# Kernel optimization log

Hardware: AMD Instinct MI355X
Metric: run time of the kernel (lower is better)

Reference implementation:

```python
import jax, jax.numpy as jnp
import numpy as np

N = 100000      # nodes
E = 1600000     # edges (before self loops)
H = 64          # hidden channels (per-head out dim, concat=False)
HEADS = 2
L = 2           # num GAT blocks
IN = 64
OUT = 10
B = 64          # graphs in batch
SLOPE = 0.2     # LeakyReLU negative slope (GATv2Conv default)
EPS = 1e-5      # BatchNorm eps


def setup_inputs() -> dict:
    key = jax.random.key(0)
    ks = jax.random.split(key, 10)
    s = 0.05
    x = jax.random.normal(ks[0], (N, IN), jnp.float32)
    edge_index = jax.random.randint(ks[1], (2, E), 0, N, dtype=jnp.int64)
    batch = jnp.sort(jax.random.randint(ks[2], (N,), 0, B, dtype=jnp.int64))
    W_enc = jax.random.normal(ks[3], (IN, H), jnp.float32) * s
    b_enc = jnp.zeros((H,), jnp.float32)
    Wl = jax.random.normal(ks[4], (L, H, HEADS * H), jnp.float32) * s
    bl = jnp.zeros((L, HEADS * H), jnp.float32)
    Wr = jax.random.normal(ks[5], (L, H, HEADS * H), jnp.float32) * s
    br = jnp.zeros((L, HEADS * H), jnp.float32)
    att = jax.random.normal(ks[6], (L, HEADS, H), jnp.float32) * s
    bias = jnp.zeros((L, H), jnp.float32)
    gamma = jnp.ones((L, H), jnp.float32)
    beta = jnp.zeros((L, H), jnp.float32)
    W_cls = jax.random.normal(ks[7], (H, OUT), jnp.float32) * s
    b_cls = jnp.zeros((OUT,), jnp.float32)
    return dict(x=x, edge_index=edge_index, batch=batch, W_enc=W_enc, b_enc=b_enc,
                Wl=Wl, bl=bl, Wr=Wr, br=br, att=att, bias=bias,
                gamma=gamma, beta=beta, W_cls=W_cls, b_cls=b_cls)


def reference(x, edge_index, batch, W_enc, b_enc, Wl, bl, Wr, br, att, bias,
              gamma, beta, W_cls, b_cls):
    # add self loops (GATv2Conv default add_self_loops=True)
    loops = jnp.arange(N, dtype=edge_index.dtype)
    ei = jnp.concatenate([edge_index, jnp.stack([loops, loops])], axis=1)
    src, dst = ei[0], ei[1]

    h = x @ W_enc + b_enc                                   # [N, H] atom encoder (Linear)
    for l in range(L):
        xl = (h @ Wl[l] + bl[l]).reshape(N, HEADS, H)       # source transform
        xr = (h @ Wr[l] + br[l]).reshape(N, HEADS, H)       # target transform
        # GATv2: e_uv = a^T LeakyReLU(W_l x_u + W_r x_v)
        z = jax.nn.leaky_relu(xl[src] + xr[dst], SLOPE)     # [E', heads, H]
        e = jnp.einsum('ehc,hc->eh', z, att[l])             # [E', heads]
        # segment softmax over incoming edges of each dst node
        m = jax.ops.segment_max(e, dst, num_segments=N)     # [N, heads]
        ex = jnp.exp(e - m[dst])
        den = jax.ops.segment_sum(ex, dst, num_segments=N)
        alpha = ex / den[dst]                               # [E', heads]
        out = jax.ops.segment_sum(xl[src] * alpha[:, :, None], dst, num_segments=N)
        h_new = out.mean(axis=1) + bias[l]                  # concat=False: mean over heads
        # BatchNorm1d (batch statistics) -> ReLU; dropout=0
        mu = h_new.mean(axis=0)
        var = h_new.var(axis=0)
        h = jax.nn.relu((h_new - mu) * jax.lax.rsqrt(var + EPS) * gamma[l] + beta[l])

    # global mean pool over graphs
    cnt = jax.ops.segment_sum(jnp.ones((N,), h.dtype), batch, num_segments=B)
    g = jax.ops.segment_sum(h, batch, num_segments=B) / jnp.maximum(cnt, 1.0)[:, None]
    return g @ W_cls + b_cls                                # [B, OUT]
```

## Files before the change

kernel.cpp:

```cpp
#include <hip/hip_runtime.h>

#define N_NODES 100000
#define E_EDGES 1600000
#define EP_EDGES (E_EDGES + N_NODES)
#define SLOPE 0.2f
#define BN_EPS 1e-5f
#define NB 8
#define NODES_PER_B 12500
#define NREP 32
#define SUBREG 8192
#define SCATTER_BLKS ((EP_EDGES + 255) / 256)
#define NBLK ((N_NODES + 63) / 64)

typedef _Float16 h2 __attribute__((ext_vector_type(2)));
typedef _Float16 v4h __attribute__((ext_vector_type(4)));
typedef _Float16 v8h __attribute__((ext_vector_type(8)));
typedef float v4f __attribute__((ext_vector_type(4)));

#if defined(__has_builtin)
#if __has_builtin(__builtin_amdgcn_fdot2)
#define HAVE_FDOT2 1
#endif
#endif

__device__ __forceinline__ float fdot2f(h2 a, h2 b, float c) {
#ifdef HAVE_FDOT2
    return __builtin_amdgcn_fdot2(a, b, c, false);
#else
    return c + (float)a[0] * (float)b[0] + (float)a[1] * (float)b[1];
#endif
}
__device__ __forceinline__ h2 bch2(unsigned u) { return __builtin_bit_cast(h2, u); }
__device__ __forceinline__ unsigned bcu(h2 v) { return __builtin_bit_cast(unsigned, v); }
__device__ __forceinline__ h2 habs2(h2 z) {
    return __builtin_bit_cast(h2, (unsigned)(__builtin_bit_cast(unsigned, z) & 0x7fff7fffu));
}
__device__ __forceinline__ h2 shflx_h2(h2 a, int o) {
    return __builtin_bit_cast(h2, __shfl_xor(__builtin_bit_cast(int, a), o, 64));
}

template <int CTRL>
__device__ __forceinline__ float dpp_add_step(float v) {
    int r = __builtin_amdgcn_update_dpp(0, __float_as_int(v), CTRL, 0xF, 0xF, false);
    return v + __int_as_float(r);
}
__device__ __forceinline__ float rowsum16(float v) {
    v = dpp_add_step<0x128>(v);
    v = dpp_add_step<0x124>(v);
    v = dpp_add_step<0x122>(v);
    v = dpp_add_step<0x121>(v);
    return v;
}

__device__ __forceinline__ void bucket_scatter_body(int bid, const int* __restrict__ src,
                                                    const int* __restrict__ dst,
                                                    int* __restrict__ gcur, unsigned* __restrict__ ebuf) {
    int i = bid * 256 + threadIdx.x;
    int rep = bid & (NREP - 1);
    bool active = i < EP_EDGES;
    int s = 0, d = 0;
    if (i < E_EDGES) { s = src[i]; d = dst[i]; }
    else if (active) { s = i - E_EDGES; d = s; }
    int b = active ? (int)((unsigned)d / NODES_PER_B) : NB;
    unsigned long long lt = (1ull << (threadIdx.x & 63)) - 1ull;
    int rank = 0;
    unsigned long long mymask = 0;
#pragma unroll
    for (int bb = 0; bb < NB; ++bb) {
        unsigned long long m = __ballot(b == bb);
        if (b == bb) { rank = __popcll(m & lt); mymask = m; }
    }
    int leader = mymask ? (__ffsll((long long)mymask) - 1) : 0;
    int lanebit = threadIdx.x & 63;
    int chunkbase = 0;
    if (active && lanebit == leader)
        chunkbase = atomicAdd(&gcur[rep * NB + b], (int)__popcll(mymask));
    chunkbase = __shfl(chunkbase, leader, 64);
    if (active) {
        unsigned dl = (unsigned)d - (unsigned)b * NODES_PER_B;
        ebuf[(size_t)(rep * NB + b) * SUBREG + chunkbase + rank] = (dl << 17) | (unsigned)s;
    }
}

__device__ __forceinline__ void fuse_enc_pack0(const float* __restrict__ We, const float* __restrict__ be,
                                               const float* __restrict__ Wl, const float* __restrict__ bl,
                                               const float* __restrict__ Wr, const float* __restrict__ br,
                                               _Float16* __restrict__ Wfrag0, float* __restrict__ bias0,
                                               float (*sWe)[64], float* sbe) {
    int t = threadIdx.x;
    for (int i = t; i < 4096; i += 256) sWe[i & 63][i >> 6] = We[i];
    if (t < 64) sbe[t] = be[t];
    __syncthreads();
    int j = t & 127, side = t >> 7;
    const float* W  = side ? Wr : Wl;
    const float* bb = side ? br : bl;
    float acc[64];
#pragma unroll
    for (int k = 0; k < 64; ++k) acc[k] = 0.f;
    float bacc = bb[j];
    for (int m = 0; m < 64; ++m) {
        float wv = W[m * 128 + j];
        bacc += sbe[m] * wv;
#pragma unroll
        for (int k = 0; k < 64; ++k) acc[k] += sWe[m][k] * wv;
    }
    int ncolg = (side << 7) | j;
    int w = ncolg >> 6, nt = (ncolg >> 4) & 3, lp = ncolg & 15;
#pragma unroll
    for (int k = 0; k < 64; ++k) {
        int kt = k >> 5;
        int l = (((k >> 3) & 3) << 4) | lp;
        int jj = k & 7;
        Wfrag0[((((w * 4 + nt) * 2 + kt)) << 9) + (l << 3) + jj] = (_Float16)acc[k];
    }
    bias0[ncolg] = bacc;
}

__device__ __forceinline__ void pack1_body(const float* __restrict__ WL, const float* __restrict__ WR,
                                           const float* __restrict__ bL, const float* __restrict__ bR,
                                           _Float16* __restrict__ Wfrag, float* __restrict__ bias_all) {
    int t = threadIdx.x;
    for (int i = t; i < 16384; i += 256) {
        int j = i & 7, l = (i >> 3) & 63, kt = (i >> 9) & 1, nt = (i >> 10) & 3, w = i >> 12;
        int ncol = w * 64 + nt * 16 + (l & 15);
        int k = kt * 32 + (l >> 4) * 8 + j;
        int side = ncol >> 7, colW = ncol & 127;
        Wfrag[i] = (_Float16)((side ? WR : WL)[k * 128 + colW]);
    }
    if (t < 256) {
        int side = t >> 7, colW = t & 127;
        bias_all[t] = (side ? bR : bL)[colW];
    }
}

__global__ __launch_bounds__(256) void scatter_fuse(const int* __restrict__ src, const int* __restrict__ dst,
                                                    int* __restrict__ gcur, unsigned* __restrict__ ebuf,
                                                    const float* __restrict__ We, const float* __restrict__ be,
                                                    const float* __restrict__ Wl, const float* __restrict__ bl,
                                                    const float* __restrict__ Wr, const float* __restrict__ br,
                                                    _Float16* __restrict__ Wfrag0, float* __restrict__ bias0,
                                                    _Float16* __restrict__ Wfrag1, float* __restrict__ bias1) {
    __shared__ float sWe[64][64];
    __shared__ float sbe[64];
    if (blockIdx.x == 0)
        fuse_enc_pack0(We, be, Wl, bl, Wr, br, Wfrag0, bias0, sWe, sbe);
    else if (blockIdx.x == 1)
        pack1_body(Wl + 64 * 128, Wr + 64 * 128, bl + 128, br + 128, Wfrag1, bias1);
    else
        bucket_scatter_body(blockIdx.x - 2, src, dst, gcur, ebuf);
}

template <int BN>
__device__ __forceinline__ void mfma_body(int mb, const void* __restrict__ hin,
                                          const _Float16* __restrict__ Wfrag,
                                          const float* __restrict__ bias_all,
                                          const float* __restrict__ bns, const float* __restrict__ gamma,
                                          const float* __restrict__ beta,
                                          unsigned short* __restrict__ xl, unsigned short* __restrict__ xr,
                                          char* smem, float* ssc, float* ssh) {
    int t = threadIdx.x;
    int w = t >> 6, l = t & 63;
    if (BN) {
        if (t < 64) {
            float s = 0.f, sq = 0.f;
#pragma unroll
            for (int r = 0; r < 8; ++r) { s += bns[r * 128 + t]; sq += bns[r * 128 + 64 + t]; }
            float mu = s * (1.f / N_NODES);
            float var = sq * (1.f / N_NODES) - mu * mu;
            float sc = gamma[t] * rsqrtf(var + BN_EPS);
            ssc[t] = sc; ssh[t] = beta[t] - mu * sc;
        }
        __syncthreads();
    }
    int base = mb * 64;
    if (BN == 0) {
#pragma unroll
        for (int pass = 0; pass < 4; ++pass) {
            int idx = t + pass * 256;
            int node = idx >> 4, q4 = idx & 15;
            int gnode = base + node;
            float4 v = make_float4(0.f, 0.f, 0.f, 0.f);
            if (gnode < N_NODES) v = *(const float4*)((const float*)hin + (size_t)gnode * 64 + q4 * 4);
            v4h p = {(_Float16)v.x, (_Float16)v.y, (_Float16)v.z, (_Float16)v.w};
            int byte = (node * 128 + q4 * 8) ^ ((node & 7) << 4);
            *(v4h*)(smem + byte) = p;
        }
    } else {
#pragma unroll
        for (int pass = 0; pass < 2; ++pass) {
            int idx = t + pass * 256;
            int node = idx >> 3, q8 = idx & 7;
            int gnode = base + node;
            uint4 u = make_uint4(0, 0, 0, 0);
            if (gnode < N_NODES) u = *(const uint4*)((const unsigned short*)hin + (size_t)gnode * 64 + q8 * 8);
            int c0 = q8 * 8;
            h2 p0 = bch2(u.x), p1 = bch2(u.y), p2 = bch2(u.z), p3 = bch2(u.w);
            float a, b;
            a = fmaxf((float)p0[0] * ssc[c0 + 0] + ssh[c0 + 0], 0.f);
            b = fmaxf((float)p0[1] * ssc[c0 + 1] + ssh[c0 + 1], 0.f);
            p0 = (h2){(_Float16)a, (_Float16)b};
            a = fmaxf((float)p1[0] * ssc[c0 + 2] + ssh[c0 + 2], 0.f);
            b = fmaxf((float)p1[1] * ssc[c0 + 3] + ssh[c0 + 3], 0.f);
            p1 = (h2){(_Float16)a, (_Float16)b};
            a = fmaxf((float)p2[0] * ssc[c0 + 4] + ssh[c0 + 4], 0.f);
            b = fmaxf((float)p2[1] * ssc[c0 + 5] + ssh[c0 + 5], 0.f);
            p2 = (h2){(_Float16)a, (_Float16)b};
            a = fmaxf((float)p3[0] * ssc[c0 + 6] + ssh[c0 + 6], 0.f);
            b = fmaxf((float)p3[1] * ssc[c0 + 7] + ssh[c0 + 7], 0.f);
            p3 = (h2){(_Float16)a, (_Float16)b};
            int byte = (node * 128 + q8 * 16) ^ ((node & 7) << 4);
            *(uint4*)(smem + byte) = make_uint4(bcu(p0), bcu(p1), bcu(p2), bcu(p3));
        }
    }
    v8h bfr[4][2];
    float biasv[4];
#pragma unroll
    for (int nt = 0; nt < 4; ++nt) {
#pragma unroll
        for (int kt = 0; kt < 2; ++kt)
            bfr[nt][kt] = *(const v8h*)(Wfrag + ((((w * 4 + nt) * 2 + kt) << 9) + (l << 3)));
        biasv[nt] = bias_all[w * 64 + nt * 16 + (l & 15)];
    }
    __syncthreads();
    v4f acc[4][4];
#pragma unroll
    for (int mt = 0; mt < 4; ++mt)
#pragma unroll
        for (int nt = 0; nt < 4; ++nt)
            acc[mt][nt] = (v4f){0.f, 0.f, 0.f, 0.f};
#pragma unroll
    for (int mt = 0; mt < 4; ++mt) {
        int node = mt * 16 + (l & 15);
        int swz = (node & 7) << 4;
        int b0 = (node * 128 + ((l >> 4) << 4)) ^ swz;
        int b1 = (node * 128 + 64 + ((l >> 4) << 4)) ^ swz;
        v8h a0 = *(const v8h*)(smem + b0);
        v8h a1 = *(const v8h*)(smem + b1);
#pragma unroll
        for (int nt = 0; nt < 4; ++nt) {
            acc[mt][nt] = __builtin_amdgcn_mfma_f32_16x16x32_f16(a0, bfr[nt][0], acc[mt][nt], 0, 0, 0);
            acc[mt][nt] = __builtin_amdgcn_mfma_f32_16x16x32_f16(a1, bfr[nt][1], acc[mt][nt], 0, 0, 0);
        }
    }
    _Float16* sOut = (_Float16*)(smem + 8192);
    __syncthreads();
#pragma unroll
    for (int mt = 0; mt < 4; ++mt) {
#pragma unroll
        for (int nt = 0; nt < 4; ++nt) {
            int ncol = (w << 6) + (nt << 4) + (l & 15);
            int side = ncol >> 7, head = (ncol >> 6) & 1, c = ncol & 63;
            int oidx = ((c >> 2) << 3) + (head << 2) + (c & 3);
            int obase = side * 128 + oidx;
#pragma unroll
            for (int j = 0; j < 4; ++j) {
                int node = mt * 16 + ((l >> 4) << 2) + j;
                sOut[node * 256 + obase] = (_Float16)(acc[mt][nt][j] + biasv[nt]);
            }
        }
    }
    __syncthreads();
#pragma unroll
    for (int pass = 0; pass < 8; ++pass) {
        int idx = t + pass * 256;
        int node = idx >> 5, wi = idx & 31;
        int gnode = base + node;
        if (gnode < N_NODES) {
            int side = wi >> 4, o16 = wi & 15;
            uint4 val = *(const uint4*)(sOut + node * 256 + side * 128 + o16 * 8);
            unsigned short* dstp = side ? xr : xl;
            *(uint4*)(dstp + (size_t)gnode * 128 + o16 * 8) = val;
        }
    }
}

__global__ __launch_bounds__(256) void deg_mfma0(const int* __restrict__ gcur,
                                                 const unsigned* __restrict__ ebuf,
                                                 int* __restrict__ deg,
                                                 const float* __restrict__ x,
                                                 const _Float16* __restrict__ Wfrag0,
                                                 const float* __restrict__ bias0,
                                                 unsigned short* __restrict__ xl, unsigned short* __restrict__ xr) {
    __shared__ __align__(16) char smem[40960];
    __shared__ float ssc[64], ssh[64];
    if (blockIdx.x < NREP * NB) {
        unsigned* ldeg4 = (unsigned*)smem;
        int b = blockIdx.x & (NB - 1), rep = blockIdx.x >> 3;
        for (int j = threadIdx.x; j < NODES_PER_B / 4 + 1; j += 256) ldeg4[j] = 0;
        __syncthreads();
        int cnt = gcur[rep * NB + b];
        int base = b * NODES_PER_B;
        const unsigned* p = ebuf + (size_t)(rep * NB + b) * SUBREG;
        for (int i = threadIdx.x; i < cnt; i += 256) {
            unsigned dl = p[i] >> 17;
            atomicAdd(&ldeg4[dl >> 2], 1u << ((dl & 3) * 8));
        }
        __syncthreads();
        for (int j = threadIdx.x; j < NODES_PER_B; j += 256) {
            unsigned v = (ldeg4[j >> 2] >> ((j & 3) * 8)) & 0xffu;
            if (v) atomicAdd(&deg[base + j], (int)v);
        }
    } else {
        mfma_body<0>(blockIdx.x - NREP * NB, x, Wfrag0, bias0, nullptr, nullptr, nullptr,
                     xl, xr, smem, ssc, ssh);
    }
}

__global__ __launch_bounds__(256) void mfma1(const unsigned short* __restrict__ hin,
                                             const _Float16* __restrict__ Wfrag1,
                                             const float* __restrict__ bias1,
                                             const float* __restrict__ bns, const float* __restrict__ gamma,
                                             const float* __restrict__ beta,
                                             unsigned short* __restrict__ xl, unsigned short* __restrict__ xr) {
    __shared__ __align__(16) char smem[40960];
    __shared__ float ssc[64], ssh[64];
    mfma_body<1>(blockIdx.x, hin, Wfrag1, bias1, bns, gamma, beta, xl, xr, smem, ssc, ssh);
}

__global__ __launch_bounds__(256) void bucket_fine(const int* __restrict__ gcur,
                                                   const unsigned* __restrict__ ebuf,
                                                   int* __restrict__ cursor, int* __restrict__ col) {
    int b = blockIdx.x & (NB - 1), rep = blockIdx.x >> 3;
    int cnt = gcur[rep * NB + b];
    int base = b * NODES_PER_B;
    const unsigned* p = ebuf + (size_t)(rep * NB + b) * SUBREG;
    for (int i = threadIdx.x; i < cnt; i += 256) {
        unsigned e = p[i];
        int d = base + (int)(e >> 17), s = (int)(e & 0x1FFFFu);
        int pos = atomicAdd(&cursor[d], 1);
        col[pos] = s;
    }
}

__global__ void scan_a(const int* __restrict__ deg, int* __restrict__ row_ptr, int* __restrict__ bsum) {
    __shared__ int wsum[16];
    int tid = threadIdx.x;
    int lane = tid & 63;
    int i = blockIdx.x * 1024 + tid;
    int x = (i < N_NODES) ? deg[i] : 0;
#pragma unroll
    for (int o = 1; o < 64; o <<= 1) {
        int y = __shfl_up(x, o, 64);
        if (lane >= o) x += y;
    }
    if (lane == 63) wsum[tid >> 6] = x;
    __syncthreads();
    if (tid < 16) {
        int s = wsum[tid];
#pragma unroll
        for (int o = 1; o < 16; o <<= 1) {
            int y = __shfl_up(s, o, 16);
            if (tid >= o) s += y;
        }
        wsum[tid] = s;
    }
    __syncthreads();
    int pre = (tid >= 64) ? wsum[(tid >> 6) - 1] : 0;
    int incl = x + pre;
    if (i < N_NODES) row_ptr[i + 1] = incl;
    if (tid == 1023) bsum[blockIdx.x] = incl;
}

__global__ void scan_c(int* __restrict__ cursor, int* __restrict__ row_ptr, const int* __restrict__ bsum) {
    __shared__ int sp[128];
    int t = threadIdx.x;
    if (t < 128) sp[t] = (t < 98) ? bsum[t] : 0;
    __syncthreads();
    for (int o = 1; o < 128; o <<= 1) {
        int v = (t < 128 && t >= o) ? sp[t - o] : 0;
        __syncthreads();
        if (t < 128) sp[t] += v;
        __syncthreads();
    }
    int i = blockIdx.x * 256 + t;
    if (i < N_NODES) {
        int d = cursor[i];
        int blk = i >> 10;
        int pre = blk ? sp[blk - 1] : 0;
        int incl = row_ptr[i + 1] + pre;
        row_ptr[i + 1] = incl;
        cursor[i] = incl - d;
        if (i == 0) row_ptr[0] = 0;
    }
}

__global__ __launch_bounds__(256) void aggregate(const char* __restrict__ xlb,
                                                 const uint4* __restrict__ xr4,
                                                 const int* __restrict__ row_ptr, const int* __restrict__ col,
                                                 const float* __restrict__ att_l, const float* __restrict__ bias_l,
                                                 unsigned short* __restrict__ hn16, float* __restrict__ bnsum) {
    int lane = threadIdx.x & 63, wid = threadIdx.x >> 6;
    int q = lane >> 4, k = lane & 15;
    int koff = k << 4;
    h2 atA0 = {(_Float16)att_l[4 * k], (_Float16)att_l[4 * k + 1]};
    h2 atA1 = {(_Float16)att_l[4 * k + 2], (_Float16)att_l[4 * k + 3]};
    h2 atB0 = {(_Float16)att_l[64 + 4 * k], (_Float16)att_l[64 + 4 * k + 1]};
    h2 atB1 = {(_Float16)att_l[64 + 4 * k + 2], (_Float16)att_l[64 + 4 * k + 3]};
    float bi0 = bias_l[4 * k], bi1 = bias_l[4 * k + 1], bi2 = bias_l[4 * k + 2], bi3 = bias_l[4 * k + 3];
    const h2 c06 = {(_Float16)0.6f, (_Float16)0.6f};
    const h2 c04 = {(_Float16)0.4f, (_Float16)0.4f};
    float ps[4] = {0, 0, 0, 0}, pq[4] = {0, 0, 0, 0};
    int w = blockIdx.x * 4 + wid, nw = gridDim.x * 4;
    for (int v = w; v < N_NODES; v += nw) {
        uint4 rp = xr4[(size_t)v * 16 + k];
        h2 rA0 = bch2(rp.x), rA1 = bch2(rp.y), rB0 = bch2(rp.z), rB1 = bch2(rp.w);
        int beg = row_ptr[v], end = row_ptr[v + 1];
        float s0 = 0.f, s1 = 0.f;
        h2 aA0 = {0, 0}, aA1 = {0, 0}, aB0 = {0, 0}, aB1 = {0, 0};
        const int* cptr = col + beg + q;
        int cv0 = cptr[0], cv1 = cptr[4], cv2 = cptr[8], cv3 = cptr[12];
        cptr += 16;
        uint4 lp0 = *(const uint4*)(xlb + (((size_t)(unsigned)cv0) << 8) + koff);
        uint4 lp1 = lp0, lp2 = lp0;
        if (beg + 4 < end) lp1 = *(const uint4*)(xlb + (((size_t)(unsigned)cv1) << 8) + koff);
        if (beg + 8 < end) lp2 = *(const uint4*)(xlb + (((size_t)(unsigned)cv2) << 8) + koff);
#pragma unroll 2
        for (int i = beg; i < end; i += 4) {
            uint4 lp3 = lp2;
            if (i + 12 < end) lp3 = *(const uint4*)(xlb + (((size_t)(unsigned)cv3) << 8) + koff);
            cv3 = *cptr; cptr += 4;
            h2 lA0 = bch2(lp0.x), lA1 = bch2(lp0.y), lB0 = bch2(lp0.z), lB1 = bch2(lp0.w);
            h2 zA0 = lA0 + rA0, zA1 = lA1 + rA1, zB0 = lB0 + rB0, zB1 = lB1 + rB1;
            h2 yA0 = zA0 * c06 + habs2(zA0) * c04;
            h2 yA1 = zA1 * c06 + habs2(zA1) * c04;
            h2 yB0 = zB0 * c06 + habs2(zB0) * c04;
            h2 yB1 = zB1 * c06 + habs2(zB1) * c04;
            float t0 = fdot2f(yA1, atA1, fdot2f(yA0, atA0, 0.f));
            float t1 = fdot2f(yB1, atB1, fdot2f(yB0, atB0, 0.f));
            t0 = rowsum16(t0); t1 = rowsum16(t1);
            bool valid = (i + q) < end;
            float p0 = valid ? __expf(t0) : 0.f;
            float p1 = valid ? __expf(t1) : 0.f;
            s0 += p0; s1 += p1;
            h2 p0h = {(_Float16)p0, (_Float16)p0};
            h2 p1h = {(_Float16)p1, (_Float16)p1};
            aA0 += p0h * lA0; aA1 += p0h * lA1;
            aB0 += p1h * lB0; aB1 += p1h * lB1;
            lp0 = lp1; lp1 = lp2; lp2 = lp3;
        }
#pragma unroll
        for (int o = 16; o <= 32; o <<= 1) {
            s0 += __shfl_xor(s0, o, 64); s1 += __shfl_xor(s1, o, 64);
            aA0 += shflx_h2(aA0, o); aA1 += shflx_h2(aA1, o);
            aB0 += shflx_h2(aB0, o); aB1 += shflx_h2(aB1, o);
        }
        if (q == 0) {
            float i0 = 0.5f / s0, i1 = 0.5f / s1;
            float hv0 = (float)aA0[0] * i0 + (float)aB0[0] * i1 + bi0;
            float hv1 = (float)aA0[1] * i0 + (float)aB0[1] * i1 + bi1;
            float hv2 = (float)aA1[0] * i0 + (float)aB1[0] * i1 + bi2;
            float hv3 = (float)aA1[1] * i0 + (float)aB1[1] * i1 + bi3;
            h2 o01 = {(_Float16)hv0, (_Float16)hv1};
            h2 o23 = {(_Float16)hv2, (_Float16)hv3};
            *(uint2*)(hn16 + (size_t)v * 64 + 4 * k) = make_uint2(bcu(o01), bcu(o23));
            ps[0] += hv0; pq[0] += hv0 * hv0;
            ps[1] += hv1; pq[1] += hv1 * hv1;
            ps[2] += hv2; pq[2] += hv2 * hv2;
            ps[3] += hv3; pq[3] += hv3 * hv3;
        }
    }
    __shared__ float sb[2][4][64];
    if (q == 0) {
#pragma unroll
        for (int j = 0; j < 4; ++j) { sb[0][wid][4 * k + j] = ps[j]; sb[1][wid][4 * k + j] = pq[j]; }
    }
    __syncthreads();
    float* dstb = bnsum + (size_t)(blockIdx.x & 7) * 128;
    int t = threadIdx.x;
    if (t < 64)
        atomicAdd(&dstb[t], sb[0][0][t] + sb[0][1][t] + sb[0][2][t] + sb[0][3][t]);
    else if (t < 128)
        atomicAdd(&dstb[t], sb[1][0][t - 64] + sb[1][1][t - 64] + sb[1][2][t - 64] + sb[1][3][t - 64]);
}

__global__ __launch_bounds__(256) void pool2(const unsigned short* __restrict__ hn,
                                             const int* __restrict__ batch,
                                             const float* __restrict__ bns, const float* __restrict__ gamma,
                                             const float* __restrict__ beta,
                                             float* __restrict__ gpool, float* __restrict__ gcnt) {
    __shared__ float ssc[64], ssh[64];
    int t = threadIdx.x;
    if (t < 64) {
        float s = 0.f, sq = 0.f;
#pragma unroll
        for (int r = 0; r < 8; ++r) { s += bns[r * 128 + t]; sq += bns[r * 128 + 64 + t]; }
        float mu = s * (1.f / N_NODES);
        float var = sq * (1.f / N_NODES) - mu * mu;
        float sc = gamma[t] * rsqrtf(var + BN_EPS);
        ssc[t] = sc; ssh[t] = beta[t] - mu * sc;
    }
    __syncthreads();
    int g = blockIdx.x >> 2, part = blockIdx.x & 3;
    int lo = 0, hi = N_NODES;
    while (lo < hi) { int mid = (lo + hi) >> 1; if (batch[mid] < g) lo = mid + 1; else hi = mid; }
    int lo2 = lo, hi2 = N_NODES;
    while (lo2 < hi2) { int mid = (lo2 + hi2) >> 1; if (batch[mid] < g + 1) lo2 = mid + 1; else hi2 = mid; }
    int len = lo2 - lo;
    if (part == 0 && t == 0) gcnt[g] = (float)len;
    int n0 = lo + (len * part) / 4, n1 = lo + (len * (part + 1)) / 4;
    int c = t & 63, r = t >> 6;
    float sc = ssc[c], sh = ssh[c];
    float acc = 0.f;
    for (int node = n0 + r; node < n1; node += 4) {
        float hv = (float)__builtin_bit_cast(_Float16, hn[(size_t)node * 64 + c]);
        acc += fmaxf(hv * sc + sh, 0.f);
    }
    __shared__ float sb[4][64];
    sb[r][c] = acc;
    __syncthreads();
    if (r == 0)
        atomicAdd(&gpool[g * 64 + c], sb[0][c] + sb[1][c] + sb[2][c] + sb[3][c]);
}

__global__ void classify(const float* __restrict__ gpool, const float* __restrict__ gcnt,
                         const float* __restrict__ Wc, const float* __restrict__ bc, float* __restrict__ out) {
    int t = threadIdx.x;
    if (t >= 640) return;
    int b = t / 10, o = t % 10;
    float inv = 1.f / fmaxf(gcnt[b], 1.f);
    float acc = 0.f;
    for (int c = 0; c < 64; ++c) acc += gpool[b * 64 + c] * Wc[c * 10 + o];
    out[t] = acc * inv + bc[o];
}

extern "C" void kernel_launch(void* const* d_in, const int* in_sizes, int n_in,
                              void* d_out, int out_size, void* d_ws, size_t ws_size,
                              hipStream_t stream) {
    (void)in_sizes; (void)n_in; (void)out_size; (void)ws_size;
    const float* x     = (const float*)d_in[0];
    const int*   ei    = (const int*)d_in[1];
    const int*   batch = (const int*)d_in[2];
    const float* W_enc = (const float*)d_in[3];
    const float* b_enc = (const float*)d_in[4];
    const float* Wl    = (const float*)d_in[5];
    const float* bl    = (const float*)d_in[6];
    const float* Wr    = (const float*)d_in[7];
    const float* br    = (const float*)d_in[8];
    const float* att   = (const float*)d_in[9];
    const float* bias  = (const float*)d_in[10];
    const float* gamma = (const float*)d_in[11];
    const float* beta  = (const float*)d_in[12];
    const float* Wc    = (const float*)d_in[13];
    const float* bc    = (const float*)d_in[14];
    float* out = (float*)d_out;

    char* ws = (char*)d_ws;
    size_t off = 0;
    auto A = [&](size_t bytes) { size_t r = off; off += (bytes + 255) & ~(size_t)255; return r; };

    int* row_ptr = (int*)(ws + A((N_NODES + 1) * 4));
    size_t colv_off = A((size_t)EP_EDGES * 4 + 426240);
    int* colv = (int*)(ws + colv_off);
    char* zbase = ws + colv_off + (size_t)EP_EDGES * 4;
    int*   cursor = (int*)(zbase + 128);
    int*   gcur   = (int*)(zbase + 400128);
    float* bns    = (float*)(zbase + 401152);
    float* gpool  = (float*)(zbase + 409344);
    float* gcnt   = (float*)(zbase + 425728);
    const size_t ZBYTES = 426240;

    unsigned short* hn    = (unsigned short*)(ws + A((size_t)N_NODES * 64 * 2));
    unsigned short* h2buf = (unsigned short*)(ws + A((size_t)N_NODES * 64 * 2));
    unsigned short* xl = (unsigned short*)(ws + A((size_t)N_NODES * 128 * 2));
    unsigned short* xr = (unsigned short*)(ws + A((size_t)N_NODES * 128 * 2));
    unsigned* ebuf = (unsigned*)(ws + A((size_t)NREP * NB * SUBREG * 4));
    int* bsum  = (int*)(ws + A(512));
    _Float16* Wfrag0 = (_Float16*)(ws + A(16384 * 2));
    _Float16* Wfrag1 = (_Float16*)(ws + A(16384 * 2));
    float* bias0 = (float*)(ws + A(256 * 4));
    float* bias1 = (float*)(ws + A(256 * 4));

    const int* srcv = ei;
    const int* dstv = ei + E_EDGES;

    hipMemsetAsync(zbase, 0, ZBYTES, stream);

    scatter_fuse<<<SCATTER_BLKS + 2, 256, 0, stream>>>(srcv, dstv, gcur, ebuf,
                                                       W_enc, b_enc, Wl, bl, Wr, br,
                                                       Wfrag0, bias0, Wfrag1, bias1);
    deg_mfma0<<<NREP * NB + NBLK, 256, 0, stream>>>(gcur, ebuf, cursor,
                                                    x, Wfrag0, bias0, xl, xr);
    scan_a<<<98, 1024, 0, stream>>>(cursor, row_ptr, bsum);
    scan_c<<<(N_NODES + 255) / 256, 256, 0, stream>>>(cursor, row_ptr, bsum);
    bucket_fine<<<NREP * NB, 256, 0, stream>>>(gcur, ebuf, cursor, colv);

    aggregate<<<4096, 256, 0, stream>>>((const char*)xl, (const uint4*)xr,
                                        row_ptr, colv, att, bias, hn, bns);
    mfma1<<<NBLK, 256, 0, stream>>>(hn, Wfrag1, bias1, bns, gamma, beta, xl, xr);
    aggregate<<<4096, 256, 0, stream>>>((const char*)xl, (const uint4*)xr,
                                        row_ptr, colv, att + 128, bias + 64, h2buf, bns + 1024);

    pool2<<<256, 256, 0, stream>>>(h2buf, batch, bns + 1024, gamma + 64, beta + 64, gpool, gcnt);
    classify<<<1, 640, 0, stream>>>(gpool, gcnt, Wc, bc, out);
}
```

Before: 365.4 us.

## Prefetch next node's row data in aggregate, use exp2, fuse classify into pool

The aggregate loop now loads the next node's row_ptr, xr row and first column indices while the current node's edges are being processed, to hide their dependent-load latency. The attention vector is pre-scaled by log2(e) so the softmax can use exp2 directly instead of __expf. The separate classify launch is folded into the pool kernel, where the last block (found with an atomic counter) computes the final output. The prefetch adds register pressure, and the last-block pattern relies on threadfence ordering.

```diff
diff --git a/kernel.cpp b/kernel.cpp
--- a/kernel.cpp
+++ b/kernel.cpp
@@ -392,28 +392,43 @@
     int lane = threadIdx.x & 63, wid = threadIdx.x >> 6;
     int q = lane >> 4, k = lane & 15;
     int koff = k << 4;
-    h2 atA0 = {(_Float16)att_l[4 * k], (_Float16)att_l[4 * k + 1]};
-    h2 atA1 = {(_Float16)att_l[4 * k + 2], (_Float16)att_l[4 * k + 3]};
-    h2 atB0 = {(_Float16)att_l[64 + 4 * k], (_Float16)att_l[64 + 4 * k + 1]};
-    h2 atB1 = {(_Float16)att_l[64 + 4 * k + 2], (_Float16)att_l[64 + 4 * k + 3]};
+    const float L2E = 1.442695040888963f;
+    h2 atA0 = {(_Float16)(L2E * att_l[4 * k]), (_Float16)(L2E * att_l[4 * k + 1])};
+    h2 atA1 = {(_Float16)(L2E * att_l[4 * k + 2]), (_Float16)(L2E * att_l[4 * k + 3])};
+    h2 atB0 = {(_Float16)(L2E * att_l[64 + 4 * k]), (_Float16)(L2E * att_l[64 + 4 * k + 1])};
+    h2 atB1 = {(_Float16)(L2E * att_l[64 + 4 * k + 2]), (_Float16)(L2E * att_l[64 + 4 * k + 3])};
     float bi0 = bias_l[4 * k], bi1 = bias_l[4 * k + 1], bi2 = bias_l[4 * k + 2], bi3 = bias_l[4 * k + 3];
     const h2 c06 = {(_Float16)0.6f, (_Float16)0.6f};
     const h2 c04 = {(_Float16)0.4f, (_Float16)0.4f};
     float ps[4] = {0, 0, 0, 0}, pq[4] = {0, 0, 0, 0};
     int w = blockIdx.x * 4 + wid, nw = gridDim.x * 4;
-    for (int v = w; v < N_NODES; v += nw) {
-        uint4 rp = xr4[(size_t)v * 16 + k];
+    int v = w;
+    int beg = 0, end = 0;
+    uint4 rp = make_uint4(0, 0, 0, 0);
+    int pc0 = 0, pc1 = 0, pc2 = 0, pc3 = 0;
+    if (v < N_NODES) {
+        beg = row_ptr[v]; end = row_ptr[v + 1];
+        rp = xr4[(size_t)v * 16 + k];
+        const int* cp = col + beg + q;
+        pc0 = cp[0]; pc1 = cp[4]; pc2 = cp[8]; pc3 = cp[12];
+    }
+    while (v < N_NODES) {
+        int v2 = v + nw;
+        int beg2 = 0, end2 = 0;
+        uint4 rp2 = rp;
+        if (v2 < N_NODES) {
+            beg2 = row_ptr[v2]; end2 = row_ptr[v2 + 1];
+            rp2 = xr4[(size_t)v2 * 16 + k];
+        }
         h2 rA0 = bch2(rp.x), rA1 = bch2(rp.y), rB0 = bch2(rp.z), rB1 = bch2(rp.w);
-        int beg = row_ptr[v], end = row_ptr[v + 1];
         float s0 = 0.f, s1 = 0.f;
         h2 aA0 = {0, 0}, aA1 = {0, 0}, aB0 = {0, 0}, aB1 = {0, 0};
-        const int* cptr = col + beg + q;
-        int cv0 = cptr[0], cv1 = cptr[4], cv2 = cptr[8], cv3 = cptr[12];
-        cptr += 16;
-        uint4 lp0 = *(const uint4*)(xlb + (((size_t)(unsigned)cv0) << 8) + koff);
+        const int* cptr = col + beg + q + 16;
+        int cv3 = pc3;
+        uint4 lp0 = *(const uint4*)(xlb + (((size_t)(unsigned)pc0) << 8) + koff);
         uint4 lp1 = lp0, lp2 = lp0;
-        if (beg + 4 < end) lp1 = *(const uint4*)(xlb + (((size_t)(unsigned)cv1) << 8) + koff);
-        if (beg + 8 < end) lp2 = *(const uint4*)(xlb + (((size_t)(unsigned)cv2) << 8) + koff);
+        if (beg + 4 < end) lp1 = *(const uint4*)(xlb + (((size_t)(unsigned)pc1) << 8) + koff);
+        if (beg + 8 < end) lp2 = *(const uint4*)(xlb + (((size_t)(unsigned)pc2) << 8) + koff);
 #pragma unroll 2
         for (int i = beg; i < end; i += 4) {
             uint4 lp3 = lp2;
@@ -429,14 +444,18 @@
             float t1 = fdot2f(yB1, atB1, fdot2f(yB0, atB0, 0.f));
             t0 = rowsum16(t0); t1 = rowsum16(t1);
             bool valid = (i + q) < end;
-            float p0 = valid ? __expf(t0) : 0.f;
-            float p1 = valid ? __expf(t1) : 0.f;
+            float p0 = valid ? __builtin_exp2f(t0) : 0.f;
+            float p1 = valid ? __builtin_exp2f(t1) : 0.f;
             s0 += p0; s1 += p1;
             h2 p0h = {(_Float16)p0, (_Float16)p0};
             h2 p1h = {(_Float16)p1, (_Float16)p1};
             aA0 += p0h * lA0; aA1 += p0h * lA1;
             aB0 += p1h * lB0; aB1 += p1h * lB1;
             lp0 = lp1; lp1 = lp2; lp2 = lp3;
+        }
+        if (v2 < N_NODES) {
+            const int* cp2 = col + beg2 + q;
+            pc0 = cp2[0]; pc1 = cp2[4]; pc2 = cp2[8]; pc3 = cp2[12];
         }
 #pragma unroll
         for (int o = 16; o <= 32; o <<= 1) {
@@ -458,6 +477,7 @@
             ps[2] += hv2; pq[2] += hv2 * hv2;
             ps[3] += hv3; pq[3] += hv3 * hv3;
         }
+        beg = beg2; end = end2; rp = rp2; v = v2;
     }
     __shared__ float sb[2][4][64];
     if (q == 0) {
@@ -473,12 +493,15 @@
         atomicAdd(&dstb[t], sb[1][0][t - 64] + sb[1][1][t - 64] + sb[1][2][t - 64] + sb[1][3][t - 64]);
 }
 
-__global__ __launch_bounds__(256) void pool2(const unsigned short* __restrict__ hn,
-                                             const int* __restrict__ batch,
-                                             const float* __restrict__ bns, const float* __restrict__ gamma,
-                                             const float* __restrict__ beta,
-                                             float* __restrict__ gpool, float* __restrict__ gcnt) {
+__global__ __launch_bounds__(256) void pool_cls(const unsigned short* __restrict__ hn,
+                                                const int* __restrict__ batch,
+                                                const float* __restrict__ bns, const float* __restrict__ gamma,
+                                                const float* __restrict__ beta,
+                                                const float* __restrict__ Wc, const float* __restrict__ bcb,
+                                                float* __restrict__ gpool, float* __restrict__ gcnt,
+                                                int* __restrict__ pcount, float* __restrict__ out) {
     __shared__ float ssc[64], ssh[64];
+    __shared__ int lastf;
     int t = threadIdx.x;
     if (t < 64) {
         float s = 0.f, sq = 0.f;
@@ -510,17 +533,20 @@
     __syncthreads();
     if (r == 0)
         atomicAdd(&gpool[g * 64 + c], sb[0][c] + sb[1][c] + sb[2][c] + sb[3][c]);
-}
-
-__global__ void classify(const float* __restrict__ gpool, const float* __restrict__ gcnt,
-                         const float* __restrict__ Wc, const float* __restrict__ bc, float* __restrict__ out) {
-    int t = threadIdx.x;
-    if (t >= 640) return;
-    int b = t / 10, o = t % 10;
-    float inv = 1.f / fmaxf(gcnt[b], 1.f);
-    float acc = 0.f;
-    for (int c = 0; c < 64; ++c) acc += gpool[b * 64 + c] * Wc[c * 10 + o];
-    out[t] = acc * inv + bc[o];
+    __threadfence();
+    __syncthreads();
+    if (t == 0) lastf = (atomicAdd(pcount, 1) == (int)gridDim.x - 1);
+    __syncthreads();
+    if (lastf) {
+        __threadfence();
+        for (int i = t; i < 640; i += 256) {
+            int b = i / 10, o = i % 10;
+            float inv = 1.f / fmaxf(gcnt[b], 1.f);
+            float a = 0.f;
+            for (int cc = 0; cc < 64; ++cc) a += gpool[b * 64 + cc] * Wc[cc * 10 + o];
+            out[i] = a * inv + bcb[o];
+        }
+    }
 }
 
 extern "C" void kernel_launch(void* const* d_in, const int* in_sizes, int n_in,
@@ -549,7 +575,7 @@
     auto A = [&](size_t bytes) { size_t r = off; off += (bytes + 255) & ~(size_t)255; return r; };
 
     int* row_ptr = (int*)(ws + A((N_NODES + 1) * 4));
-    size_t colv_off = A((size_t)EP_EDGES * 4 + 426240);
+    size_t colv_off = A((size_t)EP_EDGES * 4 + 426496);
     int* colv = (int*)(ws + colv_off);
     char* zbase = ws + colv_off + (size_t)EP_EDGES * 4;
     int*   cursor = (int*)(zbase + 128);
@@ -557,7 +583,8 @@
     float* bns    = (float*)(zbase + 401152);
     float* gpool  = (float*)(zbase + 409344);
     float* gcnt   = (float*)(zbase + 425728);
-    const size_t ZBYTES = 426240;
+    int*   pcount = (int*)(zbase + 425984);
+    const size_t ZBYTES = 426496;
 
     unsigned short* hn    = (unsigned short*)(ws + A((size_t)N_NODES * 64 * 2));
     unsigned short* h2buf = (unsigned short*)(ws + A((size_t)N_NODES * 64 * 2));
@@ -590,6 +617,6 @@
     aggregate<<<4096, 256, 0, stream>>>((const char*)xl, (const uint4*)xr,
                                         row_ptr, colv, att + 128, bias + 64, h2buf, bns + 1024);
 
-    pool2<<<256, 256, 0, stream>>>(h2buf, batch, bns + 1024, gamma + 64, beta + 64, gpool, gcnt);
-    classify<<<1, 640, 0, stream>>>(gpool, gcnt, Wc, bc, out);
-}
+    pool_cls<<<256, 256, 0, stream>>>(h2buf, batch, bns + 1024, gamma + 64, beta + 64,
+                                      Wc, bc, gpool, gcnt, pcount, out);
+}
```

New measurement: 391.0 us. +7.0%, slower.
